# Performance work log

Measured on AMD Instinct MI355X. Metric: run time of the kernel, lower is better.

Reference implementation:

```python
import jax, jax.numpy as jnp
import numpy as np

B, V, C = 256, 50, 40
VOCAB, D, H, NH, T = 10000, 256, 256, 8, 1000


def setup_inputs():
    key = jax.random.key(0)
    ks = jax.random.split(key, 24)
    f = lambda k, shape, s=0.05: jax.random.normal(k, shape, jnp.float32) * s
    # nn.Embedding(vocab_size+1, d_model, padding_idx=-1): last row is the padding row (zeros)
    emb = f(ks[0], (VOCAB + 1, D), 0.1).at[VOCAB].set(0.0)
    return dict(
        input_seqs=jax.random.randint(ks[1], (B, V, C), 0, VOCAB),
        seq_time_step=jax.random.uniform(ks[2], (B, V), jnp.float32, 0.0, 365.0),
        diffusion_time_t=jax.random.randint(ks[3], (B,), 0, T),
        normal_noise=jax.random.normal(ks[4], (B, V, D), jnp.float32),
        predicted_noise=jax.random.normal(ks[5], (B, V, D), jnp.float32),
        emb=emb,
        betas=jnp.asarray(np.linspace(1e-4, 0.02, T, dtype=np.float32)),
        tl_w=f(ks[6], (64, 1), 0.5), tl_b=f(ks[7], (64,), 0.1),
        tu_w=f(ks[8], (D, 64)), tu_b=f(ks[9], (D,), 0.01),
        in_proj_w=f(ks[10], (3 * D, D)), in_proj_b=f(ks[11], (3 * D,), 0.01),
        out_proj_w=f(ks[12], (D, D)), out_proj_b=f(ks[13], (D,), 0.01),
        w_ih=f(ks[14], (4 * H, D)), w_hh=f(ks[15], (4 * H, H)),
        b_ih=f(ks[16], (4 * H,), 0.01), b_hh=f(ks[17], (4 * H,), 0.01),
        c1_w=f(ks[18], (4 * H, H)), c1_b=f(ks[19], (4 * H,), 0.01),
        c2_w=f(ks[20], (4 * H, 4 * H)), c2_b=f(ks[21], (4 * H,), 0.01),
        co_w=f(ks[22], (2, 4 * H)), co_b=f(ks[23], (2,), 0.01),
    )


def _mha(q, kv, wi, bi, wo, bo):
    # torch MultiheadAttention on 2-D inputs -> unbatched; 'sequence length' = batch dim B
    hd = D // NH
    qp = (q @ wi[:D].T + bi[:D]).reshape(-1, NH, hd)
    kp = (kv @ wi[D:2 * D].T + bi[D:2 * D]).reshape(-1, NH, hd)
    vp = (kv @ wi[2 * D:].T + bi[2 * D:]).reshape(-1, NH, hd)
    s = jnp.einsum('qhd,khd->hqk', qp, kp) * (hd ** -0.5)
    o = jnp.einsum('hqk,khd->qhd', jax.nn.softmax(s, -1), vp).reshape(-1, D)
    return o @ wo.T + bo


def _lstm_final(seq, w_ih, w_hh, b_ih, b_hh):
    # unbatched nn.LSTM over the batch axis (length B). The original's try-branch always
    # raises (seq_h squeezed to 1-D), so the zero-init except-branch runs every visit.
    xg = seq @ w_ih.T + (b_ih + b_hh)  # [B, 4H]
    def step(carry, x):
        h, c = carry
        i, fg, g, o = jnp.split(x + h @ w_hh.T, 4)
        c = jax.nn.sigmoid(fg) * c + jax.nn.sigmoid(i) * jnp.tanh(g)
        h = jax.nn.sigmoid(o) * jnp.tanh(c)
        return (h, c), None
    z = jnp.zeros((H,), seq.dtype)
    (h, _), _ = jax.lax.scan(step, (z, z), xg)
    return h  # [H]


def _classify(h, w1, b1, w2, b2, wo, bo):
    h = jax.nn.relu(h @ w1.T + b1)
    h = jax.nn.relu(h @ w2.T + b2)
    return jax.nn.softmax(h @ wo.T + bo, -1)


def reference(input_seqs, seq_time_step, diffusion_time_t, normal_noise, predicted_noise,
              emb, betas, tl_w, tl_b, tu_w, tu_b, in_proj_w, in_proj_b, out_proj_w,
              out_proj_b, w_ih, w_hh, b_ih, b_hh, c1_w, c1_b, c2_w, c2_b, co_w, co_b):
    tt = seq_time_step[..., None] / 180.0
    tenc = (1.0 - jnp.tanh((tt @ tl_w.T + tl_b) ** 2)) @ tu_w.T + tu_b  # [B,V,D]
    ve = jax.nn.relu(emb[input_seqs]).sum(-2) + tenc                     # [B,V,D]
    alpha = jnp.cumprod(1.0 - betas)[diffusion_time_t][:, None, None]
    ven = ve * jnp.sqrt(alpha) + normal_noise * jnp.sqrt(1.0 - alpha)
    gen1 = ve + (ven - predicted_noise)
    # gen2 recurrence: row i = MHA(row i-1, gen1[:,i], gen1[:,i]); row -1 is the
    # vocab_size-filled initial tensor (valid negative index, try never fails).
    def att_step(prev, kv):
        out = _mha(prev, kv, in_proj_w, in_proj_b, out_proj_w, out_proj_b)
        return out, out
    _, gen2 = jax.lax.scan(att_step, jnp.full((B, D), float(VOCAB), ve.dtype),
                           gen1.transpose(1, 0, 2))                    # [V,B,D]
    lstm = lambda s: _lstm_final(s, w_ih, w_hh, b_ih, b_hh)
    hv = jax.vmap(lstm)(ve.transpose(1, 0, 2))  # [V,H]
    hg = jax.vmap(lstm)(gen2)                   # [V,H]
    res = jnp.broadcast_to(_classify(hv, c1_w, c1_b, c2_w, c2_b, co_w, co_b)[None], (B, V, 2))
    resg = jnp.broadcast_to(_classify(hg, c1_w, c1_b, c2_w, c2_b, co_w, co_b)[None], (B, V, 2))
    return (res, resg, res[:, -1], resg[:, -1], normal_noise, predicted_noise)
```

## Files before the change

kernel.cpp:

```cpp
#include <hip/hip_runtime.h>

#define BB 256
#define VV 50
#define CC 40
#define DD 256
#define HH 256
#define NHH 8
#define TT 1000

typedef unsigned short u16;
typedef unsigned int u32;
typedef _Float16 h2v __attribute__((ext_vector_type(2)));

__device__ __forceinline__ float blf(u16 x){ union{u32 u; float f;} z; z.u=(u32)x<<16; return z.f; }
__device__ __forceinline__ float ld(const void* p, long i, int f){
  if(f) return ((const float*)p)[i];
  return blf(((const u16*)p)[i]);
}
__device__ __forceinline__ u32 packh2(float a, float b){
  union { h2v h; u32 u; } z;
  z.h = h2v{(_Float16)a, (_Float16)b};
  return z.u;
}
__device__ __forceinline__ float fdot2(u32 a, u32 b, float c){
#if __has_builtin(__builtin_amdgcn_fdot2)
  union { u32 u; h2v h; } x, y; x.u=a; y.u=b;
  return __builtin_amdgcn_fdot2(x.h, y.h, c, false);
#else
  union { u32 u; _Float16 h[2]; } x, y; x.u=a; y.u=b;
  return c + (float)x.h[0]*(float)y.h[0] + (float)x.h[1]*(float)y.h[1];
#endif
}
__device__ __forceinline__ float sigm(float x){ return 1.f/(1.f+__expf(-x)); }
__device__ __forceinline__ float tanh_fast(float x){ return 1.f - 2.f/(__expf(2.f*x)+1.f); }

__global__ void k_flag(const void* betas, int* flag){
  if(threadIdx.x==0) flag[0] = (((const u32*)betas)[0] == 0x38D1B717u) ? 1 : 0;
}

__global__ void k_prep(const void* betas, const int* fl, float* sqa, float* s1a){
  __shared__ float sp[256];
  int t = threadIdx.x;
  int f = fl[0];
  float om[4]; float p = 1.f;
  #pragma unroll
  for(int k=0;k<4;k++){ int i=t*4+k; float be=(i<TT)?ld(betas,i,f):0.f; om[k]=1.f-be; p*=om[k]; }
  sp[t]=p; __syncthreads();
  for(int off=1; off<256; off<<=1){
    float x = (t>=off) ? sp[t-off]*sp[t] : sp[t];
    __syncthreads(); sp[t]=x; __syncthreads();
  }
  float c = (t>0)? sp[t-1] : 1.f;
  #pragma unroll
  for(int k=0;k<4;k++){
    c *= om[k]; int i=t*4+k;
    if(i<TT){ sqa[i]=sqrtf(c); s1a[i]=sqrtf(fmaxf(1.f-c,0.f)); }
  }
}

__global__ void k_packT(const void* src, float* dst, int N, int K, long elemoff, const int* fl){
  int i = blockIdx.x*256 + threadIdx.x;
  int tot = N*(K>>2);
  if(i>=tot) return;
  int f = fl[0];
  int d4 = i / N, j = i - d4*N;
  long o = elemoff + (long)j*K + (d4<<2);
  float4 r; r.x=ld(src,o,f); r.y=ld(src,o+1,f); r.z=ld(src,o+2,f); r.w=ld(src,o+3,f);
  ((float4*)dst)[i] = r;
}

__global__ void k_packQO(const void* src, u32* dst, long elemoff, const int* fl){
  int i = blockIdx.x*256 + threadIdx.x;
  if(i >= 32768) return;
  int f = fl[0];
  int c2 = i >> 8, j = i & 255;
  float a = ld(src, elemoff + (long)j*256 + 2*c2,     f);
  float b = ld(src, elemoff + (long)j*256 + 2*c2 + 1, f);
  dst[(c2>>2)*1024 + j*4 + (c2&3)] = packh2(a,b);
}

__global__ void k_packW2(const void* src, u32* whhR, u32* wclQ, const int* fl){
  int i = blockIdx.x*256 + threadIdx.x;
  if(i >= 131072) return;
  int f = fl[0];
  int row = i >> 7, cp = i & 127;
  float a = ld(src, (long)row*256 + 2*cp,     f);
  float b = ld(src, (long)row*256 + 2*cp + 1, f);
  u32 v = packh2(a,b);
  int q = cp >> 5, pp = cp & 31;
  int rb = row & 127, m = row >> 7;
  int j = q*128 + rb;
  if(pp < 24){
    int idx = m*24 + pp;
    whhR[(idx>>2)*2048 + j*4 + (idx&3)] = v;
  } else {
    int h = (pp-24) >> 2, e = (pp-24) & 3;
    wclQ[((m*2+h)*512 + j)*4 + e] = v;
  }
}

__global__ void k_ve_gen1(const int* seqs, const void* sts, const int* dt,
    const void* nn, const void* pn, const void* emb, const void* tl_w, const void* tl_b,
    const float* tu4, const void* tu_b, const float* sqa, const float* s1a, const int* fl,
    float* ve, float* gen1){
  int bv = blockIdx.x; int b = bv / VV;
  int t = threadIdx.x;
  int f = fl[0];
  __shared__ float4 f4[16];
  __shared__ int idx[CC];
  float tt = ld(sts,bv,f) * (1.f/180.f);
  if(t<64){ float x = tt*ld(tl_w,t,f) + ld(tl_b,t,f); ((float*)f4)[t] = 1.f - tanhf(x*x); }
  if(t<CC) idx[t] = seqs[bv*CC+t];
  __syncthreads();
  float acc = ld(tu_b,t,f);
  const float4* tu = (const float4*)tu4;
  #pragma unroll
  for(int d4=0; d4<16; d4++){
    float4 w = tu[d4*DD + t];
    float4 fv = f4[d4];
    acc += fv.x*w.x+fv.y*w.y+fv.z*w.z+fv.w*w.w;
  }
  float s=0.f;
  for(int c=0;c<CC;c++){ float e = ld(emb,(long)idx[c]*DD + t,f); s += fmaxf(e,0.f); }
  float vev = s + acc;
  ve[bv*DD+t] = vev;
  int tb = dt[b];
  float sa=sqa[tb], s1=s1a[tb];
  gen1[bv*DD+t] = vev*(1.f+sa) + ld(nn,(long)bv*DD+t,f)*s1 - ld(pn,(long)bv*DD+t,f);
}

__global__ void k_copy(const void* nn, const void* pn, const int* fl, float* out){
  int i = blockIdx.x*256 + threadIdx.x;
  int f = fl[0];
  const int n = BB*VV*DD;
  if(i<n){ out[52224+i]=ld(nn,i,f); out[52224+n+i]=ld(pn,i,f); }
}

__global__ void k_kvproj(const float* gen1, const float* wk4, const float* wv4,
                         const void* bi, const int* fl, float* kpT, u32* vp){
  int g = blockIdx.x; int v = g>>4; int b0 = (g&15)<<4;
  int t = threadIdx.x;
  int f = fl[0];
  __shared__ float4 x4[16][64];
  for(int r=0;r<16;r++) ((float*)x4[r])[t] = gen1[((b0+r)*VV + v)*DD + t];
  __syncthreads();
  float ak[16], av[16];
  float bk = ld(bi,DD+t,f), bvv = ld(bi,2*DD+t,f);
  #pragma unroll
  for(int r=0;r<16;r++){ ak[r]=bk; av[r]=bvv; }
  const float4* wk = (const float4*)wk4;
  const float4* wv = (const float4*)wv4;
  for(int d4=0; d4<64; d4++){
    float4 k4 = wk[d4*DD+t], v4 = wv[d4*DD+t];
    #pragma unroll
    for(int r=0;r<16;r++){
      float4 xv = x4[r][d4];
      ak[r] += xv.x*k4.x + xv.y*k4.y + xv.z*k4.z + xv.w*k4.w;
      av[r] += xv.x*v4.x + xv.y*v4.y + xv.z*v4.z + xv.w*v4.w;
    }
  }
  float* kdst = kpT + (v*DD + t)*BB + b0;
  #pragma unroll
  for(int r=0;r<16;r++) kdst[r] = ak[r];
  #pragma unroll
  for(int i2=0;i2<8;i2++){
    int k2 = (b0>>1) + i2;
    vp[(size_t)v*32768 + (k2>>2)*1024 + t*4 + (k2&3)] = packh2(av[2*i2], av[2*i2+1]);
  }
}

__global__ __launch_bounds__(256) void k_mha_all(const float* kpT, const u32* vp,
    const u32* wqp, const u32* wop, const void* ipb, const void* opb, const int* fl,
    float* gen2){
  int i = blockIdx.x, t = threadIdx.x;
  int f = fl[0];
  __shared__ __align__(16) u32 wqs[32768];
  __shared__ __align__(16) u32 xp[128];
  __shared__ float q[256];
  __shared__ float s[NHH][257];
  __shared__ __align__(16) u32 sp[NHH][128];
  __shared__ __align__(16) u32 op[128];
  __shared__ float mh[NHH], rs[NHH];
  float bq = ld(ipb, t, f);
  float bo = ld(opb, t, f);
  {
    const uint4* src = (const uint4*)wqp;
    uint4* dst = (uint4*)wqs;
    #pragma unroll
    for(int c8=0;c8<32;c8++) dst[c8*256 + t] = src[c8*256 + t];
  }
  if(t < 128) xp[t] = packh2(10000.f, 10000.f);
  __syncthreads();
  const uint4* xp4 = (const uint4*)xp;
  const uint4* op4 = (const uint4*)op;
  const uint4* wq4s = (const uint4*)wqs;
  const uint4* wo4p = (const uint4*)wop;
  int hg = t>>5, ln = t&31;
  for(int v=0; v<VV; v++){
    {
      float acc = bq;
      #pragma unroll 8
      for(int c8=0;c8<32;c8++){
        uint4 xx = xp4[c8];
        uint4 ww = wq4s[c8*256 + t];
        acc = fdot2(xx.x, ww.x, acc); acc = fdot2(xx.y, ww.y, acc);
        acc = fdot2(xx.z, ww.z, acc); acc = fdot2(xx.w, ww.w, acc);
      }
      q[t] = acc;
    }
    __syncthreads();
    {
      const float* kb = kpT + (size_t)v*BB*DD;
      #pragma unroll
      for(int h=0; h<NHH; h++){
        float acc=0.f;
        #pragma unroll
        for(int d=0; d<32; d++) acc += q[h*32+d]*kb[(h*32+d)*BB + t];
        s[h][t] = acc*0.1767766952966369f;
      }
    }
    __syncthreads();
    float m=-3.0e38f;
    for(int k=ln;k<BB;k+=32) m=fmaxf(m, s[hg][k]);
    for(int off=16;off;off>>=1) m=fmaxf(m, __shfl_down(m,off,32));
    if(ln==0) mh[hg]=m;
    __syncthreads();
    #pragma unroll
    for(int h=0;h<NHH;h++) s[h][t]=__expf(s[h][t]-mh[h]);
    __syncthreads();
    float sm=0.f;
    for(int k=ln;k<BB;k+=32) sm += s[hg][k];
    for(int off=16;off;off>>=1) sm += __shfl_down(sm,off,32);
    if(ln==0) rs[hg]=1.f/sm;
    #pragma unroll
    for(int m2=t; m2<1024; m2+=256){
      int h = m2>>7, k2 = m2&127;
      sp[h][k2] = packh2(s[h][2*k2], s[h][2*k2+1]);
    }
    __syncthreads();
    {
      const uint4* vb = (const uint4*)(vp + (size_t)v*32768);
      const uint4* spv = (const uint4*)sp[hg];
      float acc = 0.f;
      #pragma unroll 8
      for(int k8=0;k8<32;k8++){
        uint4 pv = spv[k8];
        uint4 vv = vb[k8*256 + t];
        acc = fdot2(pv.x, vv.x, acc); acc = fdot2(pv.y, vv.y, acc);
        acc = fdot2(pv.z, vv.z, acc); acc = fdot2(pv.w, vv.w, acc);
      }
      float o = acc * rs[hg];
      float oo = __shfl_xor(o, 1, 64);
      if((t&1)==0) op[t>>1] = packh2(o, oo);
    }
    __syncthreads();
    {
      float acc = bo;
      #pragma unroll 8
      for(int c8=0;c8<32;c8++){
        uint4 xx = op4[c8];
        uint4 ww = wo4p[c8*256 + t];
        acc = fdot2(xx.x, ww.x, acc); acc = fdot2(xx.y, ww.y, acc);
        acc = fdot2(xx.z, ww.z, acc); acc = fdot2(xx.w, ww.w, acc);
      }
      gen2[((size_t)v*BB+i)*DD + t] = acc;
      float ax = __shfl_xor(acc, 1, 64);
      if((t&1)==0) xp[t>>1] = packh2(acc, ax);
    }
    __syncthreads();
  }
}

__global__ __launch_bounds__(256, 2) void k_xg(const float* inp, int is_ve, const float* wih4,
                     const void* b_ih, const void* b_hh, const int* fl, u16* xg){
  int g = blockIdx.x; int v=g>>4; int b0=(g&15)<<4;
  int t = threadIdx.x;
  int f = fl[0];
  __shared__ float4 x4[16][64];
  for(int r=0;r<16;r++){
    int b = b0+r;
    const float* src = is_ve ? (inp + (b*VV+v)*DD) : (inp + (v*BB+b)*DD);
    ((float*)x4[r])[t] = src[t];
  }
  __syncthreads();
  float acc[4][16];
  #pragma unroll
  for(int js=0;js<4;js++){
    float bsum = ld(b_ih,js*256+t,f) + ld(b_hh,js*256+t,f);
    #pragma unroll
    for(int r=0;r<16;r++) acc[js][r]=bsum;
  }
  const float4* wf = (const float4*)wih4;
  #pragma unroll 2
  for(int d4=0; d4<64; d4++){
    float4 w[4];
    #pragma unroll
    for(int js=0;js<4;js++) w[js] = wf[d4*1024 + js*256 + t];
    #pragma unroll
    for(int r=0;r<16;r++){
      float4 xv = x4[r][d4];
      #pragma unroll
      for(int js=0;js<4;js++)
        acc[js][r] += xv.x*w[js].x+xv.y*w[js].y+xv.z*w[js].z+xv.w*w[js].w;
    }
  }
  for(int r=0;r<16;r++)
    #pragma unroll
    for(int js=0;js<4;js++){
      union { _Float16 h; u16 u; } z;
      z.h = (_Float16)acc[js][r];
      xg[(size_t)(v*BB + b0 + r)*1024 + js*256 + t] = z.u;
    }
}

__global__ __attribute__((amdgpu_flat_work_group_size(512,512)))
__attribute__((amdgpu_waves_per_eu(2,2)))
void k_lstm3(const u16* xgA, const u16* xgB,
    const u32* whhR, const u32* wclQ, float* hfin){
  int b = blockIdx.x, j = threadIdx.x;
  int q = j >> 7, rb = j & 127;
  const u16* xgv = (b < VV) ? (xgA + (size_t)b*BB*1024) : (xgB + (size_t)(b-VV)*BB*1024);
  __shared__ __align__(16) u32 wcl[32768];
  __shared__ __align__(16) float pacc[4][1024];
  __shared__ __align__(16) u32 hp[128];
  u32 w[192];
  { const uint4* wr4 = (const uint4*)whhR;
    #pragma unroll
    for(int i4=0;i4<48;i4++){
      uint4 v = wr4[i4*512 + j];
      w[i4*4+0]=v.x; w[i4*4+1]=v.y; w[i4*4+2]=v.z; w[i4*4+3]=v.w;
    } }
  {
    const uint4* src = (const uint4*)wclQ;
    uint4* dst = (uint4*)wcl;
    #pragma unroll
    for(int i=0;i<16;i++) dst[i*512 + j] = src[i*512 + j];
  }
  if(j < 128) hp[j] = 0u;
  float c0 = 0.f, h_t = 0.f;
  __syncthreads();
  const uint4* hp4 = (const uint4*)hp;
  const uint4* wcl4 = (const uint4*)wcl;
  for(int s=0; s<BB; s++){
    asm volatile("" ::: "memory");
    u16 nx0=0,nx1=0,nx2=0,nx3=0;
    if(j < 256){
      nx0 = xgv[s*1024 +       j];
      nx1 = xgv[s*1024 + 256 + j];
      nx2 = xgv[s*1024 + 512 + j];
      nx3 = xgv[s*1024 + 768 + j];
    }
    float acc[8];
    #pragma unroll
    for(int m=0;m<8;m++) acc[m]=0.f;
    #pragma unroll
    for(int i=0;i<6;i++){
      uint4 hh = hp4[q*8 + i];
      #pragma unroll
      for(int m=0;m<8;m++){
        acc[m] = fdot2(hh.x, w[m*24 + i*4+0], acc[m]);
        acc[m] = fdot2(hh.y, w[m*24 + i*4+1], acc[m]);
        acc[m] = fdot2(hh.z, w[m*24 + i*4+2], acc[m]);
        acc[m] = fdot2(hh.w, w[m*24 + i*4+3], acc[m]);
      }
    }
    #pragma unroll
    for(int h=0;h<2;h++){
      uint4 hh = hp4[q*8 + 6 + h];
      #pragma unroll
      for(int m=0;m<8;m++){
        uint4 s4 = wcl4[(m*2+h)*512 + j];
        acc[m] = fdot2(hh.x, s4.x, acc[m]);
        acc[m] = fdot2(hh.y, s4.y, acc[m]);
        acc[m] = fdot2(hh.z, s4.z, acc[m]);
        acc[m] = fdot2(hh.w, s4.w, acc[m]);
      }
    }
    #pragma unroll
    for(int m=0;m<8;m++) pacc[q][m*128 + rb] = acc[m];
    __syncthreads();
    if(j < 256){
      float a0 = pacc[0][      j] + pacc[1][      j] + pacc[2][      j] + pacc[3][      j];
      float a1 = pacc[0][256 + j] + pacc[1][256 + j] + pacc[2][256 + j] + pacc[3][256 + j];
      float a2 = pacc[0][512 + j] + pacc[1][512 + j] + pacc[2][512 + j] + pacc[3][512 + j];
      float a3 = pacc[0][768 + j] + pacc[1][768 + j] + pacc[2][768 + j] + pacc[3][768 + j];
      float ai = a0 + (float)(*(const _Float16*)&nx0);
      float af = a1 + (float)(*(const _Float16*)&nx1);
      float ag = a2 + (float)(*(const _Float16*)&nx2);
      float ao = a3 + (float)(*(const _Float16*)&nx3);
      float ig = sigm(ai), fg = sigm(af), og = sigm(ao);
      float gg = tanh_fast(ag);
      c0 = fg*c0 + ig*gg;
      h_t = og*tanh_fast(c0);
      float ho = __shfl_xor(h_t, 1, 64);
      if((j&1)==0) hp[j>>1] = packh2(h_t, ho);
    }
    __syncthreads();
  }
  if(j < 256) hfin[b*HH + j] = h_t;
}

__global__ void k_cls(const float* hfin, const float* c14, const void* c1b,
                      const float* c24, const void* c2b, const void* cow, const void* cob,
                      const int* fl, float* cls){
  int blk = blockIdx.x;
  int t = threadIdx.x;
  int f = fl[0];
  __shared__ float4 h4[64];
  __shared__ float4 h14[256];
  __shared__ float4 h24[256];
  __shared__ float red0[4], red1[4];
  ((float*)h4)[t] = hfin[blk*HH + t];
  __syncthreads();
  {
    float a[4];
    #pragma unroll
    for(int js=0;js<4;js++) a[js]=ld(c1b,js*256+t,f);
    const float4* wf = (const float4*)c14;
    for(int d4=0; d4<64; d4++){
      float4 hv = h4[d4];
      #pragma unroll
      for(int js=0;js<4;js++){
        float4 w = wf[d4*1024 + js*256+t];
        a[js] += hv.x*w.x+hv.y*w.y+hv.z*w.z+hv.w*w.w;
      }
    }
    #pragma unroll
    for(int js=0;js<4;js++) ((float*)h14)[js*256+t] = fmaxf(a[js],0.f);
  }
  __syncthreads();
  {
    float a[4];
    #pragma unroll
    for(int js=0;js<4;js++) a[js]=ld(c2b,js*256+t,f);
    const float4* wf = (const float4*)c24;
    for(int d4=0; d4<256; d4++){
      float4 hv = h14[d4];
      #pragma unroll
      for(int js=0;js<4;js++){
        float4 w = wf[d4*1024 + js*256+t];
        a[js] += hv.x*w.x+hv.y*w.y+hv.z*w.z+hv.w*w.w;
      }
    }
    #pragma unroll
    for(int js=0;js<4;js++) ((float*)h24)[js*256+t] = fmaxf(a[js],0.f);
  }
  __syncthreads();
  float p0=0.f,p1=0.f;
  #pragma unroll
  for(int js=0;js<4;js++){
    int j=js*256+t;
    float hv=((float*)h24)[j];
    p0 += hv*ld(cow,j,f);
    p1 += hv*ld(cow,1024+j,f);
  }
  for(int off=32;off;off>>=1){ p0+=__shfl_down(p0,off,64); p1+=__shfl_down(p1,off,64); }
  if((t&63)==0){ red0[t>>6]=p0; red1[t>>6]=p1; }
  __syncthreads();
  if(t==0){
    float l0 = ld(cob,0,f) + red0[0]+red0[1]+red0[2]+red0[3];
    float l1 = ld(cob,1,f) + red1[0]+red1[1]+red1[2]+red1[3];
    float mm = fmaxf(l0,l1);
    float e0=__expf(l0-mm), e1=__expf(l1-mm);
    float inv = 1.f/(e0+e1);
    cls[blk*2] = e0*inv; cls[blk*2+1] = e1*inv;
  }
}

__global__ void k_out(const float* cls, float* out){
  int i = blockIdx.x*256 + threadIdx.x;
  if(i < BB*VV*2){
    int v = (i>>1) % VV, k = i&1;
    out[i] = cls[v*2+k];
    out[BB*VV*2 + i] = cls[(VV+v)*2+k];
  }
  if(i < BB*2){
    int k=i&1;
    out[2*BB*VV*2 + i]        = cls[(VV-1)*2+k];
    out[2*BB*VV*2 + BB*2 + i] = cls[(2*VV-1)*2+k];
  }
}

extern "C" void kernel_launch(void* const* d_in, const int* in_sizes, int n_in,
                              void* d_out, int out_size, void* d_ws, size_t ws_size,
                              hipStream_t stream){
  const int* seqs = (const int*)d_in[0];
  const void* sts  = d_in[1];
  const int* dt   = (const int*)d_in[2];
  const void* nn   = d_in[3];
  const void* pn   = d_in[4];
  const void* emb  = d_in[5];
  const void* betas= d_in[6];
  const void* tl_w = d_in[7];
  const void* tl_b = d_in[8];
  const void* tu_w = d_in[9];
  const void* tu_b = d_in[10];
  const void* ipw  = d_in[11];
  const void* ipb  = d_in[12];
  const void* opw  = d_in[13];
  const void* opb  = d_in[14];
  const void* wih  = d_in[15];
  const void* whh  = d_in[16];
  const void* bih  = d_in[17];
  const void* bhh  = d_in[18];
  const void* c1w  = d_in[19];
  const void* c1b  = d_in[20];
  const void* c2w  = d_in[21];
  const void* c2b  = d_in[22];
  const void* cow  = d_in[23];
  const void* cob  = d_in[24];

  char* base = (char*)d_ws;
  float* wk4  = (float*)(base + 0);
  float* wv4  = (float*)(base + 262144);
  u32*   wqp  = (u32*)(base + 524288);
  u32*   wop  = (u32*)(base + 655360);
  float* wih4 = (float*)(base + 786432);
  u32*   whhR = (u32*)(base + 1835008);
  u32*   wclQ = (u32*)(base + 2228224);
  float* c14  = (float*)(base + 2359296);
  float* c24  = (float*)(base + 3407872);
  float* tu4  = (float*)(base + 7602176);
  float* sqa  = (float*)(base + 7667712);
  float* s1a  = (float*)(base + 7671808);
  float* hfin = (float*)(base + 7675904);
  float* cls  = (float*)(base + 7778304);
  int*   flag = (int*)(base + 7779328);
  float* ve   = (float*)(base + 7783424);
  float* g12  = (float*)(base + 20890624);
  char*  arena= base + 33997824;
  float* kpT  = (float*)(arena);
  u32*   vp   = (u32*)(arena + 13107200);
  u16*   xgA  = (u16*)(arena);
  u16*   xgB  = (u16*)(arena + 26214400);
  float* out  = (float*)d_out;

  k_flag<<<1,64,0,stream>>>(betas, flag);
  k_prep<<<1,256,0,stream>>>(betas, flag, sqa, s1a);
  k_packT<<<64,256,0,stream>>>(ipw,  wk4, 256, 256, 65536L,  flag);
  k_packT<<<64,256,0,stream>>>(ipw,  wv4, 256, 256, 131072L, flag);
  k_packQO<<<128,256,0,stream>>>(ipw, wqp, 0, flag);
  k_packQO<<<128,256,0,stream>>>(opw, wop, 0, flag);
  k_packT<<<256,256,0,stream>>>(wih, wih4,1024, 256, 0, flag);
  k_packW2<<<512,256,0,stream>>>(whh, whhR, wclQ, flag);
  k_packT<<<256,256,0,stream>>>(c1w, c14, 1024, 256, 0, flag);
  k_packT<<<1024,256,0,stream>>>(c2w,c24, 1024,1024, 0, flag);
  k_packT<<<16,256,0,stream>>>(tu_w, tu4, 256, 64, 0, flag);

  k_ve_gen1<<<BB*VV,256,0,stream>>>(seqs,sts,dt,nn,pn,emb,tl_w,tl_b,tu4,tu_b,sqa,s1a,flag,ve,g12);
  k_copy<<<(BB*VV*DD+255)/256,256,0,stream>>>(nn,pn,flag,out);

  k_kvproj<<<VV*16,256,0,stream>>>(g12, wk4, wv4, ipb, flag, kpT, vp);
  k_mha_all<<<BB,256,0,stream>>>(kpT, vp, wqp, wop, ipb, opb, flag, g12);

  k_xg<<<VV*16,256,0,stream>>>(ve,  1, wih4, bih, bhh, flag, xgA);
  k_xg<<<VV*16,256,0,stream>>>(g12, 0, wih4, bih, bhh, flag, xgB);
  k_lstm3<<<100,512,0,stream>>>(xgA, xgB, whhR, wclQ, hfin);

  k_cls<<<2*VV,256,0,stream>>>(hfin, c14, c1b, c24, c2b, cow, cob, flag, cls);
  k_out<<<100,256,0,stream>>>(cls, out);
}
```

Measured before the change: 1.800 ms.

## Split MHA recurrence reductions across 512 threads with shared-memory partial sums

The per-batch attention recurrence kernel now runs 512 threads instead of 256. Each half computes partial dot products over half of the reduction dimension for the Q projection, attention-value product and output projection, and the halves are combined through shared memory. The softmax exp and sum are also fused into a single pass using 64-lane wavefront reductions. This shortens the serial chain in each of the 50 dependent steps at the cost of extra barriers and shared-memory traffic per step.

```diff
diff --git a/kernel.cpp b/kernel.cpp
--- a/kernel.cpp
+++ b/kernel.cpp
@@ -169,25 +169,27 @@
   }
 }
 
-__global__ __launch_bounds__(256) void k_mha_all(const float* kpT, const u32* vp,
+__global__ __launch_bounds__(512) void k_mha_all(const float* kpT, const u32* vp,
     const u32* wqp, const u32* wop, const void* ipb, const void* opb, const int* fl,
     float* gen2){
   int i = blockIdx.x, t = threadIdx.x;
+  int tl = t & 255, th = t >> 8;
   int f = fl[0];
   __shared__ __align__(16) u32 wqs[32768];
   __shared__ __align__(16) u32 xp[128];
-  __shared__ float q[256];
+  __shared__ float qp2[2][256];
   __shared__ float s[NHH][257];
   __shared__ __align__(16) u32 sp[NHH][128];
+  __shared__ float opp[2][256];
   __shared__ __align__(16) u32 op[128];
   __shared__ float mh[NHH], rs[NHH];
-  float bq = ld(ipb, t, f);
-  float bo = ld(opb, t, f);
+  float bq = ld(ipb, tl, f);
+  float bo = ld(opb, tl, f);
   {
     const uint4* src = (const uint4*)wqp;
     uint4* dst = (uint4*)wqs;
     #pragma unroll
-    for(int c8=0;c8<32;c8++) dst[c8*256 + t] = src[c8*256 + t];
+    for(int k=0;k<16;k++) dst[k*512 + t] = src[k*512 + t];
   }
   if(t < 128) xp[t] = packh2(10000.f, 10000.f);
   __syncthreads();
@@ -195,74 +197,93 @@
   const uint4* op4 = (const uint4*)op;
   const uint4* wq4s = (const uint4*)wqs;
   const uint4* wo4p = (const uint4*)wop;
-  int hg = t>>5, ln = t&31;
+  int hg = t>>6, ln = t&63;
+  int c0 = th*16;
   for(int v=0; v<VV; v++){
     {
-      float acc = bq;
+      float acc = th ? 0.f : bq;
       #pragma unroll 8
-      for(int c8=0;c8<32;c8++){
-        uint4 xx = xp4[c8];
-        uint4 ww = wq4s[c8*256 + t];
+      for(int c8=0;c8<16;c8++){
+        uint4 xx = xp4[c0+c8];
+        uint4 ww = wq4s[(c0+c8)*256 + tl];
         acc = fdot2(xx.x, ww.x, acc); acc = fdot2(xx.y, ww.y, acc);
         acc = fdot2(xx.z, ww.z, acc); acc = fdot2(xx.w, ww.w, acc);
       }
-      q[t] = acc;
-    }
+      qp2[th][tl] = acc;
+    }
+    __syncthreads();
+    if(t < 256) qp2[0][t] += qp2[1][t];
     __syncthreads();
     {
       const float* kb = kpT + (size_t)v*BB*DD;
-      #pragma unroll
-      for(int h=0; h<NHH; h++){
-        float acc=0.f;
+      const float* qq = qp2[0];
+      #pragma unroll
+      for(int hh=0; hh<4; hh++){
+        int h = th*4 + hh;
+        float acc = 0.f;
         #pragma unroll
-        for(int d=0; d<32; d++) acc += q[h*32+d]*kb[(h*32+d)*BB + t];
-        s[h][t] = acc*0.1767766952966369f;
+        for(int d=0; d<32; d++) acc += qq[h*32+d]*kb[(h*32+d)*BB + tl];
+        s[h][tl] = acc*0.1767766952966369f;
       }
     }
     __syncthreads();
     float m=-3.0e38f;
-    for(int k=ln;k<BB;k+=32) m=fmaxf(m, s[hg][k]);
-    for(int off=16;off;off>>=1) m=fmaxf(m, __shfl_down(m,off,32));
+    #pragma unroll
+    for(int k=ln;k<BB;k+=64) m=fmaxf(m, s[hg][k]);
+    #pragma unroll
+    for(int off=32;off;off>>=1) m=fmaxf(m, __shfl_down(m,off,64));
     if(ln==0) mh[hg]=m;
     __syncthreads();
-    #pragma unroll
-    for(int h=0;h<NHH;h++) s[h][t]=__expf(s[h][t]-mh[h]);
-    __syncthreads();
-    float sm=0.f;
-    for(int k=ln;k<BB;k+=32) sm += s[hg][k];
-    for(int off=16;off;off>>=1) sm += __shfl_down(sm,off,32);
-    if(ln==0) rs[hg]=1.f/sm;
-    #pragma unroll
-    for(int m2=t; m2<1024; m2+=256){
+    {
+      float mv = mh[hg];
+      float sm=0.f;
+      #pragma unroll
+      for(int k=ln;k<BB;k+=64){ float e=__expf(s[hg][k]-mv); s[hg][k]=e; sm+=e; }
+      #pragma unroll
+      for(int off=32;off;off>>=1) sm += __shfl_down(sm,off,64);
+      if(ln==0) rs[hg]=1.f/sm;
+    }
+    __syncthreads();
+    #pragma unroll
+    for(int m2=t; m2<1024; m2+=512){
       int h = m2>>7, k2 = m2&127;
       sp[h][k2] = packh2(s[h][2*k2], s[h][2*k2+1]);
     }
     __syncthreads();
     {
       const uint4* vb = (const uint4*)(vp + (size_t)v*32768);
-      const uint4* spv = (const uint4*)sp[hg];
+      const uint4* spv = (const uint4*)sp[tl>>5];
       float acc = 0.f;
       #pragma unroll 8
-      for(int k8=0;k8<32;k8++){
-        uint4 pv = spv[k8];
-        uint4 vv = vb[k8*256 + t];
+      for(int k8=0;k8<16;k8++){
+        uint4 pv = spv[c0+k8];
+        uint4 vv = vb[(c0+k8)*256 + tl];
         acc = fdot2(pv.x, vv.x, acc); acc = fdot2(pv.y, vv.y, acc);
         acc = fdot2(pv.z, vv.z, acc); acc = fdot2(pv.w, vv.w, acc);
       }
-      float o = acc * rs[hg];
+      opp[th][tl] = acc;
+    }
+    __syncthreads();
+    if(t < 256){
+      float o = (opp[0][t] + opp[1][t]) * rs[t>>5];
       float oo = __shfl_xor(o, 1, 64);
       if((t&1)==0) op[t>>1] = packh2(o, oo);
     }
     __syncthreads();
     {
-      float acc = bo;
+      float acc = th ? 0.f : bo;
       #pragma unroll 8
-      for(int c8=0;c8<32;c8++){
-        uint4 xx = op4[c8];
-        uint4 ww = wo4p[c8*256 + t];
+      for(int c8=0;c8<16;c8++){
+        uint4 xx = op4[c0+c8];
+        uint4 ww = wo4p[(c0+c8)*256 + tl];
         acc = fdot2(xx.x, ww.x, acc); acc = fdot2(xx.y, ww.y, acc);
         acc = fdot2(xx.z, ww.z, acc); acc = fdot2(xx.w, ww.w, acc);
       }
+      opp[th][tl] = acc;
+    }
+    __syncthreads();
+    if(t < 256){
+      float acc = opp[0][t] + opp[1][t];
       gen2[((size_t)v*BB+i)*DD + t] = acc;
       float ax = __shfl_xor(acc, 1, 64);
       if((t&1)==0) xp[t>>1] = packh2(acc, ax);
@@ -551,7 +572,7 @@
   k_copy<<<(BB*VV*DD+255)/256,256,0,stream>>>(nn,pn,flag,out);
 
   k_kvproj<<<VV*16,256,0,stream>>>(g12, wk4, wv4, ipb, flag, kpT, vp);
-  k_mha_all<<<BB,256,0,stream>>>(kpT, vp, wqp, wop, ipb, opb, flag, g12);
+  k_mha_all<<<BB,512,0,stream>>>(kpT, vp, wqp, wop, ipb, opb, flag, g12);
 
   k_xg<<<VV*16,256,0,stream>>>(ve,  1, wih4, bih, bhh, flag, xgA);
   k_xg<<<VV*16,256,0,stream>>>(g12, 0, wih4, bih, bhh, flag, xgB);
```

Result: slower. 2.308 ms (+28.3%).

## Store K projection as packed fp16 and stage it in LDS per step

Applied to the files above, without the earlier changes.

The K projection is now written as packed half2 values in an interleaved layout instead of transposed fp32. The attention kernel copies each step's K block into shared memory with async global-to-LDS loads and computes scores with fdot2. To free shared memory for this, the Q weights are read from global memory instead of being cached in LDS. This halves K traffic and replaces scalar FMAs with packed dot products, at the cost of fp16 precision for K and Q and repeated global reads of Wq.

```diff
diff --git a/kernel.cpp b/kernel.cpp
--- a/kernel.cpp
+++ b/kernel.cpp
@@ -137,7 +137,7 @@
 }
 
 __global__ void k_kvproj(const float* gen1, const float* wk4, const float* wv4,
-                         const void* bi, const int* fl, float* kpT, u32* vp){
+                         const void* bi, const int* fl, u32* kpHq, u32* vp){
   int g = blockIdx.x; int v = g>>4; int b0 = (g&15)<<4;
   int t = threadIdx.x;
   int f = fl[0];
@@ -159,9 +159,12 @@
       av[r] += xv.x*v4.x + xv.y*v4.y + xv.z*v4.z + xv.w*v4.w;
     }
   }
-  float* kdst = kpT + (v*DD + t)*BB + b0;
-  #pragma unroll
-  for(int r=0;r<16;r++) kdst[r] = ak[r];
+  #pragma unroll
+  for(int r=0;r<16;r++){
+    float a2 = __shfl_xor(ak[r], 1, 64);
+    if((t&1)==0)
+      kpHq[(size_t)v*32768 + (t>>3)*1024 + (size_t)(b0+r)*4 + ((t>>1)&3)] = packh2(ak[r], a2);
+  }
   #pragma unroll
   for(int i2=0;i2<8;i2++){
     int k2 = (b0>>1) + i2;
@@ -169,53 +172,71 @@
   }
 }
 
-__global__ __launch_bounds__(256) void k_mha_all(const float* kpT, const u32* vp,
+__global__ __launch_bounds__(256) void k_mha_all(const u32* kpHq, const u32* vp,
     const u32* wqp, const u32* wop, const void* ipb, const void* opb, const int* fl,
     float* gen2){
   int i = blockIdx.x, t = threadIdx.x;
   int f = fl[0];
-  __shared__ __align__(16) u32 wqs[32768];
+  __shared__ __align__(16) u32 kls[32768];
   __shared__ __align__(16) u32 xp[128];
-  __shared__ float q[256];
+  __shared__ __align__(16) u32 qpp[128];
   __shared__ float s[NHH][257];
   __shared__ __align__(16) u32 sp[NHH][128];
   __shared__ __align__(16) u32 op[128];
   __shared__ float mh[NHH], rs[NHH];
   float bq = ld(ipb, t, f);
   float bo = ld(opb, t, f);
-  {
-    const uint4* src = (const uint4*)wqp;
-    uint4* dst = (uint4*)wqs;
-    #pragma unroll
-    for(int c8=0;c8<32;c8++) dst[c8*256 + t] = src[c8*256 + t];
-  }
   if(t < 128) xp[t] = packh2(10000.f, 10000.f);
   __syncthreads();
   const uint4* xp4 = (const uint4*)xp;
   const uint4* op4 = (const uint4*)op;
-  const uint4* wq4s = (const uint4*)wqs;
+  const uint4* wq4p = (const uint4*)wqp;
   const uint4* wo4p = (const uint4*)wop;
+  const uint4* kls4 = (const uint4*)kls;
+  const uint4* qp4  = (const uint4*)qpp;
   int hg = t>>5, ln = t&31;
   for(int v=0; v<VV; v++){
+    {
+      const u32* kg = kpHq + (size_t)v*32768;
+#if __has_builtin(__builtin_amdgcn_global_load_lds)
+      #pragma unroll
+      for(int j=0;j<32;j++){
+        __builtin_amdgcn_global_load_lds(
+          (const __attribute__((address_space(1))) u32*)(kg + (j*256 + t)*4),
+          (__attribute__((address_space(3))) u32*)(kls + (j*256 + t)*4), 16, 0, 0);
+      }
+#else
+      const uint4* kg4 = (const uint4*)kg;
+      uint4* kl4 = (uint4*)kls;
+      #pragma unroll 8
+      for(int j=0;j<32;j++) kl4[j*256+t] = kg4[j*256+t];
+#endif
+    }
     {
       float acc = bq;
       #pragma unroll 8
       for(int c8=0;c8<32;c8++){
         uint4 xx = xp4[c8];
-        uint4 ww = wq4s[c8*256 + t];
+        uint4 ww = wq4p[c8*256 + t];
         acc = fdot2(xx.x, ww.x, acc); acc = fdot2(xx.y, ww.y, acc);
         acc = fdot2(xx.z, ww.z, acc); acc = fdot2(xx.w, ww.w, acc);
       }
-      q[t] = acc;
-    }
+      float aq2 = __shfl_xor(acc, 1, 64);
+      if((t&1)==0) qpp[t>>1] = packh2(acc, aq2);
+    }
+    asm volatile("s_waitcnt vmcnt(0)" ::: "memory");
     __syncthreads();
     {
-      const float* kb = kpT + (size_t)v*BB*DD;
       #pragma unroll
       for(int h=0; h<NHH; h++){
-        float acc=0.f;
+        float acc = 0.f;
         #pragma unroll
-        for(int d=0; d<32; d++) acc += q[h*32+d]*kb[(h*32+d)*BB + t];
+        for(int dd=0; dd<4; dd++){
+          uint4 kk = kls4[(h*4+dd)*256 + t];
+          uint4 qq = qp4[h*4+dd];
+          acc = fdot2(qq.x, kk.x, acc); acc = fdot2(qq.y, kk.y, acc);
+          acc = fdot2(qq.z, kk.z, acc); acc = fdot2(qq.w, kk.w, acc);
+        }
         s[h][t] = acc*0.1767766952966369f;
       }
     }
@@ -529,7 +550,7 @@
   float* ve   = (float*)(base + 7783424);
   float* g12  = (float*)(base + 20890624);
   char*  arena= base + 33997824;
-  float* kpT  = (float*)(arena);
+  u32*   kpHq = (u32*)(arena);
   u32*   vp   = (u32*)(arena + 13107200);
   u16*   xgA  = (u16*)(arena);
   u16*   xgB  = (u16*)(arena + 26214400);
@@ -550,8 +571,8 @@
   k_ve_gen1<<<BB*VV,256,0,stream>>>(seqs,sts,dt,nn,pn,emb,tl_w,tl_b,tu4,tu_b,sqa,s1a,flag,ve,g12);
   k_copy<<<(BB*VV*DD+255)/256,256,0,stream>>>(nn,pn,flag,out);
 
-  k_kvproj<<<VV*16,256,0,stream>>>(g12, wk4, wv4, ipb, flag, kpT, vp);
-  k_mha_all<<<BB,256,0,stream>>>(kpT, vp, wqp, wop, ipb, opb, flag, g12);
+  k_kvproj<<<VV*16,256,0,stream>>>(g12, wk4, wv4, ipb, flag, kpHq, vp);
+  k_mha_all<<<BB,256,0,stream>>>(kpHq, vp, wqp, wop, ipb, opb, flag, g12);
 
   k_xg<<<VV*16,256,0,stream>>>(ve,  1, wih4, bih, bhh, flag, xgA);
   k_xg<<<VV*16,256,0,stream>>>(g12, 0, wih4, bih, bhh, flag, xgB);
```

New measurement: 1.760 ms. -2.2%, faster.
